# Kernel optimization log

Hardware: AMD Instinct MI355X
Metric: run time of the kernel (lower is better)

Reference implementation:

```python
import jax, jax.numpy as jnp
import numpy as np

N_CLASSES = 18
NMS_PRE = 1000   # test_cfg.nms_pre, per level
K_NMS = 500      # per-class candidates entering greedy NMS
SCORE_THR = 0.01
IOU_THR = 0.5
LEVEL_NS = [600000, 300000, 150000, 75000]


def _decode(points, pred):
    # fcaf3d axis-aligned decode: pred = (dx-, dx+, dy-, dy+, dz-, dz+) >= 0
    cx = points[:, 0] + (pred[:, 1] - pred[:, 0]) / 2
    cy = points[:, 1] + (pred[:, 3] - pred[:, 2]) / 2
    cz = points[:, 2] + (pred[:, 5] - pred[:, 4]) / 2
    w = pred[:, 0] + pred[:, 1]
    l = pred[:, 2] + pred[:, 3]
    h = pred[:, 4] + pred[:, 5]
    return jnp.stack([cx, cy, cz, w, l, h], axis=-1)  # [N, 6]


def _iou3d(b):
    # axis-aligned 3D IoU, b: [K,6] (cx,cy,cz,w,l,h) -> [K,K]
    mn = b[:, :3] - b[:, 3:] / 2
    mx = b[:, :3] + b[:, 3:] / 2
    lt = jnp.maximum(mn[:, None, :], mn[None, :, :])
    rb = jnp.minimum(mx[:, None, :], mx[None, :, :])
    inter = jnp.clip(rb - lt, 0.0).prod(-1)
    vol = jnp.clip(mx - mn, 0.0).prod(-1)
    return inter / (vol[:, None] + vol[None, :] - inter + 1e-6)


def _level(centerness, bbox_pred, cls_score, points):
    # fused score: cls.sigmoid() * centerness.sigmoid()
    scores = jax.nn.sigmoid(cls_score) * jax.nn.sigmoid(centerness)  # [N,C]
    max_scores = scores.max(axis=1)
    _, ids = jax.lax.top_k(max_scores, NMS_PRE)  # per-level prefilter
    bboxes = _decode(points[ids], bbox_pred[ids])  # [NMS_PRE, 6]
    return bboxes, scores[ids]


def _nms_class(boxes, scores):
    # boxes [M,6], scores [M] for one class -> greedy NMS on top K_NMS
    valid = scores > SCORE_THR
    s = jnp.where(valid, scores, -1.0)
    sv, order = jax.lax.top_k(s, K_NMS)  # sorted desc
    b = boxes[order]
    v = sv > SCORE_THR
    iou = _iou3d(b)  # [K,K]
    idx = jnp.arange(K_NMS)

    def body(i, sup):
        alive = jnp.logical_not(sup[i])
        return sup | (alive & (iou[i] > IOU_THR) & (idx > i))

    sup = jax.lax.fori_loop(0, K_NMS, body, jnp.logical_not(v))
    keep = jnp.logical_not(sup) & v
    return b, sv, keep


def _forward(levels):
    mlvl_bboxes, mlvl_scores = [], []
    for (cn, bp, cs, pt) in levels:
        b, s = _level(cn, bp, cs, pt)
        mlvl_bboxes.append(b)
        mlvl_scores.append(s)
    bboxes = jnp.concatenate(mlvl_bboxes)  # [4*NMS_PRE, 6]
    scores = jnp.concatenate(mlvl_scores)  # [4*NMS_PRE, C]
    # per-class NMS (vmap over class dim)
    b, sv, keep = jax.vmap(_nms_class, in_axes=(None, 1))(bboxes, scores)
    labels = jnp.broadcast_to(jnp.arange(N_CLASSES, dtype=jnp.int32)[:, None], sv.shape)
    return (b.reshape(-1, 6), sv.reshape(-1), labels.reshape(-1), keep.reshape(-1))


def setup_inputs() -> dict:
    key = jax.random.key(0)
    out = {}
    for li, n in enumerate(LEVEL_NS):
        k1, k2, k3, k4, key = jax.random.split(key, 5)
        out[f'centerness{li}'] = jax.random.normal(k1, (n, 1), jnp.float32)
        out[f'bbox_pred{li}'] = jax.random.uniform(k2, (n, 6), jnp.float32)  # non-negative distances
        out[f'cls_score{li}'] = jax.random.normal(k3, (n, N_CLASSES), jnp.float32)
        out[f'points{li}'] = jax.random.normal(k4, (n, 3), jnp.float32) * 2.0
    return out


def reference(centerness0, bbox_pred0, cls_score0, points0,
              centerness1, bbox_pred1, cls_score1, points1,
              centerness2, bbox_pred2, cls_score2, points2,
              centerness3, bbox_pred3, cls_score3, points3):
    levels = [
        (centerness0, bbox_pred0, cls_score0, points0),
        (centerness1, bbox_pred1, cls_score1, points1),
        (centerness2, bbox_pred2, cls_score2, points2),
        (centerness3, bbox_pred3, cls_score3, points3),
    ]
    return _forward(levels)
```

## Files before the change

kernel.cpp:

```cpp
#include <hip/hip_runtime.h>
#include <math.h>

#define N_CLASSES 18
#define NMS_PRE   1000
#define K_NMS     500
#define POOL      4000
#define LIST_CAP  2048
#define IOU_THR   0.5f
#define SCORE_THR 0.01f

typedef unsigned long long ull;

struct Ptrs {
  const float* cent[4];
  const float* bbox[4];
  const float* cls[4];
  const float* pts[4];
  int off[4];
  int ntot;
};

__device__ __forceinline__ unsigned int fsort(float f){
  unsigned int b = __float_as_uint(f);
  return (b & 0x80000000u) ? ~b : (b | 0x80000000u);
}
__device__ __forceinline__ float fsort_inv(unsigned int k){
  unsigned int b = (k & 0x80000000u) ? (k & 0x7FFFFFFFu) : ~k;
  return __uint_as_float(b);
}
__device__ __forceinline__ float sigmoidf_(float x){
  return 1.0f / (1.0f + expf(-x));
}
__device__ __forceinline__ int level_of(int f, const Ptrs& P){
  return (f >= P.off[3]) ? 3 : (f >= P.off[2]) ? 2 : (f >= P.off[1]) ? 1 : 0;
}

__device__ __forceinline__ ull cx_keep(ull mine, ull part, bool keep_hi){
  ull mx = mine > part ? mine : part;
  ull mn = mine > part ? part : mine;
  return keep_hi ? mx : mn;
}
__device__ __forceinline__ void cxpair(ull &a, ull &b, bool a_hi){
  ull mx = a > b ? a : b;
  ull mn = a > b ? b : a;
  a = a_hi ? mx : mn;
  b = a_hi ? mn : mx;
}

__global__ void __launch_bounds__(256) init_kernel(unsigned int* hist, unsigned int* state,
                        unsigned int* cnts){
  for (int j = threadIdx.x; j < 4*2048; j += 256) hist[j] = 0u;
  if (threadIdx.x < 4){
    state[2*threadIdx.x]   = 0u;
    state[2*threadIdx.x+1] = NMS_PRE;
    cnts[threadIdx.x]      = 0u;
  }
}

__global__ void __launch_bounds__(256) compute_keys(Ptrs P, unsigned int* keys,
                        unsigned int* hist){
  __shared__ float cls_s[256*19];
  __shared__ unsigned int lh[2048];
  int t = threadIdx.x;
  for (int j = t; j < 2048; j += 256) lh[j] = 0u;
  int f0 = blockIdx.x << 8;
  int f = f0 + t;
  float m = 0.f, cent = 0.f;
  bool valid = f < P.ntot;
  int fl = min(f0 + 255, P.ntot - 1);
  bool uni = (level_of(f0, P) == level_of(fl, P)) && (f0 + 255 < P.ntot);
  int Lb = level_of(f0, P);
  if (uni){
    const float* base = P.cls[Lb] + (size_t)(f0 - P.off[Lb]) * N_CLASSES;
    const float4* base4 = (const float4*)base;
    for (int j = t; j < 256*N_CLASSES/4; j += 256){
      float4 v = base4[j];
      int e = 4*j;
      cls_s[((e  )/18)*19 + ((e  )%18)] = v.x;
      cls_s[((e+1)/18)*19 + ((e+1)%18)] = v.y;
      cls_s[((e+2)/18)*19 + ((e+2)%18)] = v.z;
      cls_s[((e+3)/18)*19 + ((e+3)%18)] = v.w;
    }
    __syncthreads();
    m = cls_s[t*19];
#pragma unroll
    for (int c = 1; c < N_CLASSES; ++c) m = fmaxf(m, cls_s[t*19 + c]);
    cent = P.cent[Lb][f - P.off[Lb]];
  } else {
    __syncthreads();
    if (valid){
      int L = level_of(f, P); int i = f - P.off[L];
      const float* cl = P.cls[L] + (size_t)i * N_CLASSES;
      m = cl[0];
      for (int c = 1; c < N_CLASSES; ++c) m = fmaxf(m, cl[c]);
      cent = P.cent[L][i];
    }
  }
  if (valid){
    float s = sigmoidf_(m) * sigmoidf_(cent);
    unsigned int key = fsort(s);
    keys[f] = key;
    unsigned int bin = key >> 21;
    if (uni) atomicAdd(&lh[bin], 1u);
    else     atomicAdd(&hist[level_of(f, P)*2048 + bin], 1u);
  }
  __syncthreads();
  if (uni){
    for (int j = t; j < 2048; j += 256){
      unsigned int v = lh[j];
      if (v) atomicAdd(&hist[Lb*2048 + j], v);
    }
  }
}

__global__ void __launch_bounds__(256) hist_level(Ptrs P, const unsigned int* keys,
                        const unsigned int* state, unsigned int* hist){
  int f = blockIdx.x * 256 + threadIdx.x;
  if (f < P.ntot){
    int L = level_of(f, P);
    unsigned int key = keys[f];
    unsigned int Pfx = state[2*L];
    if ((key >> 21) == (Pfx >> 21))
      atomicAdd(&hist[L*2048 + ((key >> 10) & 0x7FFu)], 1u);
  }
}

__global__ void __launch_bounds__(256) scan_level(unsigned int* hist, unsigned int* state, int pass){
  __shared__ unsigned int lhist[4*2048];
  int t = threadIdx.x;
  int w = t >> 6, lane = t & 63;
  for (int j = t; j < 4*2048; j += 256) lhist[j] = hist[j];
  __syncthreads();
  {
    unsigned int krem = state[2*w + 1];
    unsigned int Pfx  = state[2*w];
    unsigned int carry = 0;
    for (int ch = 0; ch < 32; ++ch){
      int d = ch*64 + lane;
      unsigned int cnt = lhist[w*2048 + (2047 - d)];
      unsigned int pfx = cnt;
#pragma unroll
      for (int off = 1; off < 64; off <<= 1){
        unsigned int u = __shfl_up(pfx, off);
        if (lane >= off) pfx += u;
      }
      unsigned int C = carry + pfx;
      ull bal = __ballot(C >= krem);
      if (bal){
        int fl2 = __ffsll(bal) - 1;
        unsigned int Cf = __shfl(C, fl2);
        unsigned int cf = __shfl(cnt, fl2);
        if (lane == 0){
          unsigned int b = (unsigned int)(2047 - (ch*64 + fl2));
          state[2*w]     = (pass == 0) ? (b << 21) : (Pfx | (b << 10));
          state[2*w + 1] = krem - (Cf - cf);
        }
        break;
      }
      carry = __shfl(C, 63);
    }
  }
  if (pass == 0){
    __syncthreads();
    for (int j = t; j < 4*2048; j += 256) hist[j] = 0u;
  }
}

__global__ void __launch_bounds__(256) compact_kernel(Ptrs P, const unsigned int* keys,
                        const unsigned int* state, unsigned int* cnts, ull* lists){
  int f = blockIdx.x * 256 + threadIdx.x;
  if (f >= P.ntot) return;
  int L = level_of(f, P);
  unsigned int key = keys[f];
  unsigned int T = state[2*L];
  if (key >= T){
    unsigned int pos = atomicAdd(&cnts[L], 1u);
    if (pos < LIST_CAP){
      unsigned int i = (unsigned int)(f - P.off[L]);
      lists[(size_t)L*LIST_CAP + pos] = ((ull)key << 32) | (ull)(~i);
    }
  }
}

__global__ void __launch_bounds__(1024) sort_idx(const ull* lists,
                        const unsigned int* cnts, unsigned int* sidx){
  __shared__ ull buf[LIST_CAP];
  int L = blockIdx.x;
  int t = threadIdx.x;
  unsigned int cnt = cnts[L]; if (cnt > LIST_CAP) cnt = LIST_CAP;
  const ull* src = lists + (size_t)L*LIST_CAP;
  if (cnt <= 1024u){
    ull v0 = (t < (int)cnt) ? src[t] : 0ull;
    for (int k = 2; k <= 1024; k <<= 1){
      for (int j = k >> 1; j > 0; j >>= 1){
        bool hi0 = (((t & j) == 0) == ((t & k) == 0));
        if (j >= 64){
          __syncthreads();
          buf[t] = v0;
          __syncthreads();
          ull p0 = buf[t ^ j];
          v0 = cx_keep(v0, p0, hi0);
        } else {
          ull p0 = __shfl_xor(v0, j);
          v0 = cx_keep(v0, p0, hi0);
        }
      }
    }
    if (t < NMS_PRE) sidx[L*NMS_PRE + t] = ~((unsigned int)(v0 & 0xFFFFFFFFu));
  } else {
    int e1 = t + 1024;
    ull v0 = (t  < (int)cnt) ? src[t]  : 0ull;
    ull v1 = (e1 < (int)cnt) ? src[e1] : 0ull;
    for (int k = 2; k <= 2048; k <<= 1){
      for (int j = k >> 1; j > 0; j >>= 1){
        bool hi0 = (((t  & j) == 0) == ((t  & k) == 0));
        bool hi1 = (((e1 & j) == 0) == ((e1 & k) == 0));
        if (j >= 1024){
          cxpair(v0, v1, hi0);
        } else if (j >= 64){
          __syncthreads();
          buf[t] = v0; buf[e1] = v1;
          __syncthreads();
          ull p0 = buf[t ^ j];
          ull p1 = buf[e1 ^ j];
          v0 = cx_keep(v0, p0, hi0);
          v1 = cx_keep(v1, p1, hi1);
        } else {
          ull p0 = __shfl_xor(v0, j);
          ull p1 = __shfl_xor(v1, j);
          v0 = cx_keep(v0, p0, hi0);
          v1 = cx_keep(v1, p1, hi1);
        }
      }
    }
    if (t < NMS_PRE) sidx[L*NMS_PRE + t] = ~((unsigned int)(v0 & 0xFFFFFFFFu));
  }
}

__global__ void __launch_bounds__(64) gather_decode(Ptrs P, const unsigned int* sidx,
                        float* boxes_pool, float* scores_pool){
  int r = blockIdx.x*64 + threadIdx.x;
  if (r >= POOL) return;
  int L = r / NMS_PRE;
  unsigned int i = sidx[r];
  const float* bp = P.bbox[L] + (size_t)i * 6;
  const float* pp = P.pts[L]  + (size_t)i * 3;
  float p0 = bp[0], p1 = bp[1], p2 = bp[2], p3 = bp[3], p4 = bp[4], p5 = bp[5];
  float cx = pp[0] + (p1 - p0) * 0.5f;
  float cy = pp[1] + (p3 - p2) * 0.5f;
  float cz = pp[2] + (p5 - p4) * 0.5f;
  float w = p0 + p1, l = p2 + p3, h = p4 + p5;
  float* bo = boxes_pool + (size_t)r * 6;
  bo[0] = cx; bo[1] = cy; bo[2] = cz; bo[3] = w; bo[4] = l; bo[5] = h;
  float cs = sigmoidf_(P.cent[L][i]);
  const float* cl = P.cls[L] + (size_t)i * N_CLASSES;
#pragma unroll
  for (int c = 0; c < N_CLASSES; ++c)
    scores_pool[(size_t)c * POOL + r] = sigmoidf_(cl[c]) * cs;
}

__global__ void __launch_bounds__(1024) class_topk(const float* scores_pool, const float* boxes_pool,
                        float* out, float* aabb){
  __shared__ unsigned int keyS[4096];
  __shared__ ull comp[512];
  __shared__ unsigned int histS[256];
  __shared__ unsigned int wsum[16], wpre[16];
  __shared__ unsigned int sP, sK, sCnt;
  int c = blockIdx.x;
  int t = threadIdx.x;
  int w = t >> 6, lane = t & 63;

  for (int j = t; j < 4096; j += 1024){
    unsigned int k = 0u;
    if (j < POOL){
      float s = scores_pool[(size_t)c*POOL + j];
      float sval = (s > SCORE_THR) ? s : -1.0f;
      k = fsort(sval);
    }
    keyS[j] = k;
  }
  if (t == 0){ sP = 0u; sK = K_NMS; sCnt = 0u; }
  __syncthreads();

  for (int pass = 0; pass < 4; ++pass){
    int shift = 24 - 8*pass;
    if (t < 256) histS[t] = 0u;
    __syncthreads();
    unsigned int Pfx = sP;
    for (int j = t; j < 4096; j += 1024){
      unsigned int k = keyS[j];
      if ((((ull)(k ^ Pfx)) >> (shift + 8)) == 0ull)
        atomicAdd(&histS[(k >> shift) & 0xFFu], 1u);
    }
    __syncthreads();
    if (w == 0){
      unsigned int krem = sK;
      unsigned int carry = 0;
      for (int ch = 0; ch < 4; ++ch){
        unsigned int cnt = histS[255 - (ch*64 + lane)];
        unsigned int pfx = cnt;
#pragma unroll
        for (int off = 1; off < 64; off <<= 1){
          unsigned int u = __shfl_up(pfx, off);
          if (lane >= off) pfx += u;
        }
        unsigned int C = carry + pfx;
        ull bal = __ballot(C >= krem);
        if (bal){
          int fl = __ffsll(bal) - 1;
          unsigned int Cf = __shfl(C, fl);
          unsigned int cf = __shfl(cnt, fl);
          if (lane == 0){
            sP = Pfx | ((unsigned int)(255 - (ch*64 + fl)) << shift);
            sK = krem - (Cf - cf);
          }
          break;
        }
        carry = __shfl(C, 63);
      }
    }
    __syncthreads();
  }
  unsigned int T = sP, need = sK;

  unsigned int loc[4]; unsigned int ct = 0;
#pragma unroll
  for (int q = 0; q < 4; ++q){
    unsigned int k = keyS[4*t + q];
    loc[q] = k;
    ct += (k == T) ? 1u : 0u;
  }
  unsigned int inc = ct;
#pragma unroll
  for (int off = 1; off < 64; off <<= 1){
    unsigned int u = __shfl_up(inc, off);
    if (lane >= off) inc += u;
  }
  if (lane == 63) wsum[w] = inc;
  __syncthreads();
  if (t < 16){
    unsigned int v = wsum[t];
    unsigned int pincl = v;
#pragma unroll
    for (int off = 1; off < 16; off <<= 1){
      unsigned int u = __shfl_up(pincl, off);
      if (t >= off) pincl += u;
    }
    wpre[t] = pincl - v;
  }
  __syncthreads();
  unsigned int excl = wpre[w] + (inc - ct);

#pragma unroll
  for (int q = 0; q < 4; ++q){
    unsigned int k = loc[q];
    bool surv = false;
    if (k > T) surv = true;
    else if (k == T){ surv = (excl < need); excl += 1u; }
    if (surv){
      unsigned int pos = atomicAdd(&sCnt, 1u);
      if (pos < 512)
        comp[pos] = ((ull)k << 32) | (ull)(~(unsigned int)(4*t + q));
    }
  }
  __syncthreads();

  ull v0 = 0ull;
  if (t < 512 && t < (int)sCnt) v0 = comp[t];
  for (int k = 2; k <= 512; k <<= 1){
    for (int j = k >> 1; j > 0; j >>= 1){
      if (j >= 64){
        __syncthreads();
        if (t < 512) comp[t] = v0;
        __syncthreads();
        if (t < 512){
          ull p0 = comp[t ^ j];
          bool hi0 = (((t & j) == 0) == ((t & k) == 0));
          v0 = cx_keep(v0, p0, hi0);
        }
      } else {
        if (t < 512){
          ull p0 = __shfl_xor(v0, j);
          bool hi0 = (((t & j) == 0) == ((t & k) == 0));
          v0 = cx_keep(v0, p0, hi0);
        }
      }
    }
  }

  if (t < K_NMS){
    ull cm = v0;
    unsigned int j = ~((unsigned int)(cm & 0xFFFFFFFFu));
    float sval = fsort_inv((unsigned int)(cm >> 32));
    int o = c*K_NMS + t;
    const float* bp = boxes_pool + (size_t)j * 6;
    float b0 = bp[0], b1 = bp[1], b2 = bp[2], b3 = bp[3], b4 = bp[4], b5 = bp[5];
    float* ob = out + (size_t)o * 6;
    ob[0] = b0; ob[1] = b1; ob[2] = b2; ob[3] = b3; ob[4] = b4; ob[5] = b5;
    out[54000 + o] = sval;
    out[63000 + o] = (float)c;
    float mn0 = b0 - b3*0.5f, mx0 = b0 + b3*0.5f;
    float mn1 = b1 - b4*0.5f, mx1 = b1 + b4*0.5f;
    float mn2 = b2 - b5*0.5f, mx2 = b2 + b5*0.5f;
    float vol = fmaxf(mx0 - mn0, 0.f) * fmaxf(mx1 - mn1, 0.f) * fmaxf(mx2 - mn2, 0.f);
    float* ap = aabb + ((size_t)c*512 + t) * 8;
    ap[0] = mn0; ap[1] = mn1; ap[2] = mn2; ap[3] = mx0; ap[4] = mx1; ap[5] = mx2;
    ap[6] = vol; ap[7] = sval;
  }
}

__global__ void __launch_bounds__(512) nms_mask(const float* aabb, ull* maskG, ull* flagsG){
  __shared__ float smn0[512], smn1[512], smn2[512];
  __shared__ float smx0[512], smx1[512], smx2[512];
  __shared__ float svol[512];
  __shared__ ull rowbuf[64*8];
  int c = blockIdx.y, chunk = blockIdx.x;
  int t = threadIdx.x, w = t >> 6, lane = t & 63;
  float mn0 = 0.f, mn1 = 0.f, mn2 = 0.f, mx0 = 0.f, mx1 = 0.f, mx2 = 0.f, vol = 0.f;
  if (t < K_NMS){
    const float* ap = aabb + ((size_t)c*512 + t) * 8;
    mn0 = ap[0]; mn1 = ap[1]; mn2 = ap[2];
    mx0 = ap[3]; mx1 = ap[4]; mx2 = ap[5]; vol = ap[6];
  }
  smn0[t] = mn0; smn1[t] = mn1; smn2[t] = mn2;
  smx0[t] = mx0; smx1[t] = mx1; smx2[t] = mx2;
  svol[t] = vol;
  __syncthreads();
  int i0 = chunk * 64, i1 = min(i0 + 64, K_NMS);
  for (int i = i0; i < i1; ++i){
    float lt0 = fmaxf(smn0[i], mn0), lt1 = fmaxf(smn1[i], mn1), lt2 = fmaxf(smn2[i], mn2);
    float rb0 = fminf(smx0[i], mx0), rb1 = fminf(smx1[i], mx1), rb2 = fminf(smx2[i], mx2);
    float inter = fmaxf(rb0 - lt0, 0.f) * fmaxf(rb1 - lt1, 0.f) * fmaxf(rb2 - lt2, 0.f);
    float denom = svol[i] + vol - inter + 1e-6f;
    bool s = (t < K_NMS) && (t > i) && (inter / denom > IOU_THR);
    ull m = __ballot(s);
    if (lane == 0){
      maskG[((size_t)c*K_NMS + i)*8 + w] = m;
      rowbuf[(i - i0)*8 + w] = m;
    }
  }
  __syncthreads();
  if (t < 64){
    int r = i0 + t;
    bool nz = false;
    if (r < K_NMS){
      ull o = 0ull;
#pragma unroll
      for (int z = 0; z < 8; ++z) o |= rowbuf[t*8 + z];
      nz = (o != 0ull);
    }
    ull bal = __ballot(nz);
    if (t == 0) flagsG[(size_t)c*8 + chunk] = bal;
  }
}

__global__ void __launch_bounds__(512) nms_greedy(const float* aabb, const ull* maskG,
                        const ull* flagsG, float* keep_out){
  __shared__ ull maskS[K_NMS*8];
  __shared__ ull vbitsS[8], remS[8];
  int c = blockIdx.x, t = threadIdx.x, w = t >> 6, lane = t & 63;
  ull flg[8];
#pragma unroll
  for (int q = 0; q < 8; ++q) flg[q] = flagsG[(size_t)c*8 + q];
  for (int j = t; j < K_NMS*8; j += 512) maskS[j] = maskG[(size_t)c*K_NMS*8 + j];
  float sv = (t < K_NMS) ? aabb[((size_t)c*512 + t)*8 + 7] : -1.0f;
  ull vb = __ballot(sv > SCORE_THR);
  if (lane == 0) vbitsS[w] = vb;
  __syncthreads();
  if (w == 0){
    ull rem[8];
#pragma unroll
    for (int q = 0; q < 8; ++q) rem[q] = ~vbitsS[q];
#pragma unroll
    for (int q = 0; q < 8; ++q){
      ull cand = flg[q] & ~rem[q];
      while (cand){
        int b = __ffsll(cand) - 1;
        int i = q*64 + b;
#pragma unroll
        for (int z = 0; z < 8; ++z) rem[z] |= maskS[i*8 + z];
        ull above = (b < 63) ? (~0ull << (b + 1)) : 0ull;
        cand = flg[q] & ~rem[q] & above;
      }
    }
    if (lane == 0){
#pragma unroll
      for (int q = 0; q < 8; ++q) remS[q] = rem[q];
    }
  }
  __syncthreads();
  if (t < K_NMS)
    keep_out[c*K_NMS + t] = ((remS[t >> 6] >> (t & 63)) & 1ull) ? 0.0f : 1.0f;
}

extern "C" void kernel_launch(void* const* d_in, const int* in_sizes, int n_in,
                              void* d_out, int out_size, void* d_ws, size_t ws_size,
                              hipStream_t stream){
  Ptrs P;
  int off = 0;
  for (int L = 0; L < 4; ++L){
    P.cent[L] = (const float*)d_in[4*L + 0];
    P.bbox[L] = (const float*)d_in[4*L + 1];
    P.cls[L]  = (const float*)d_in[4*L + 2];
    P.pts[L]  = (const float*)d_in[4*L + 3];
    P.off[L]  = off;
    off += in_sizes[4*L + 0];
  }
  P.ntot = off;

  char* w = (char*)d_ws;
  size_t o = 0;
  auto alloc = [&](size_t bytes) -> char* {
    char* p = w + o;
    o = (o + bytes + 255) & ~(size_t)255;
    return p;
  };
  unsigned int* keys        = (unsigned int*)alloc((size_t)P.ntot * 4);
  unsigned int* hist        = (unsigned int*)alloc(4 * 2048 * 4);
  unsigned int* state       = (unsigned int*)alloc(4 * 2 * 4);
  unsigned int* cnts        = (unsigned int*)alloc(4 * 4);
  ull* lists                = (ull*)alloc((size_t)4 * LIST_CAP * 8);
  unsigned int* sidx        = (unsigned int*)alloc((size_t)POOL * 4);
  float* boxes_pool         = (float*)alloc((size_t)POOL * 6 * 4);
  float* scores_pool        = (float*)alloc((size_t)N_CLASSES * POOL * 4);
  float* aabb               = (float*)alloc((size_t)N_CLASSES * 512 * 8 * 4);
  ull* maskG                = (ull*)alloc((size_t)N_CLASSES * K_NMS * 8 * 8);
  ull* flagsG               = (ull*)alloc((size_t)N_CLASSES * 8 * 8);

  float* out = (float*)d_out;
  int grid = (P.ntot + 255) / 256;

  init_kernel<<<1, 256, 0, stream>>>(hist, state, cnts);
  compute_keys<<<grid, 256, 0, stream>>>(P, keys, hist);
  scan_level<<<1, 256, 0, stream>>>(hist, state, 0);
  hist_level<<<grid, 256, 0, stream>>>(P, keys, state, hist);
  scan_level<<<1, 256, 0, stream>>>(hist, state, 1);
  compact_kernel<<<grid, 256, 0, stream>>>(P, keys, state, cnts, lists);
  sort_idx<<<4, 1024, 0, stream>>>(lists, cnts, sidx);
  gather_decode<<<(POOL + 63)/64, 64, 0, stream>>>(P, sidx, boxes_pool, scores_pool);
  class_topk<<<N_CLASSES, 1024, 0, stream>>>(scores_pool, boxes_pool, out, aabb);
  nms_mask<<<dim3(8, N_CLASSES), 512, 0, stream>>>(aabb, maskG, flagsG);
  nms_greedy<<<N_CLASSES, 512, 0, stream>>>(aabb, maskG, flagsG, out + 72000);
}
```

Baseline: 312.7 us.

## Fuse pipeline stages with last-block scans and merge NMS into class top-k kernel

Cuts the launch chain from eleven kernels to five plus a memset. The two radix-scan passes now run inside the histogram kernels, using a last-block-done atomic counter and threadfence. Gather/decode is folded into the per-level sort kernel, and the IoU mask and greedy NMS stages are merged into the per-class top-k kernel using shared memory instead of global mask buffers. compute_keys also moves to 512-thread blocks with a plain float4 copy into unpadded shared memory. The aim is to remove launch gaps and global round-trips, at the cost of serial tail work in the last block and heavier shared-memory use in class_all.

```diff
diff --git a/kernel.cpp b/kernel.cpp
--- a/kernel.cpp
+++ b/kernel.cpp
@@ -47,52 +47,65 @@
   b = a_hi ? mn : mx;
 }
 
-__global__ void __launch_bounds__(256) init_kernel(unsigned int* hist, unsigned int* state,
-                        unsigned int* cnts){
-  for (int j = threadIdx.x; j < 4*2048; j += 256) hist[j] = 0u;
-  if (threadIdx.x < 4){
-    state[2*threadIdx.x]   = 0u;
-    state[2*threadIdx.x+1] = NMS_PRE;
-    cnts[threadIdx.x]      = 0u;
-  }
-}
-
-__global__ void __launch_bounds__(256) compute_keys(Ptrs P, unsigned int* keys,
-                        unsigned int* hist){
-  __shared__ float cls_s[256*19];
-  __shared__ unsigned int lh[2048];
+__device__ __forceinline__ void level_scan(const unsigned int* st, unsigned int* state,
+                                           int pass, int w, int lane){
+  unsigned int krem = (pass == 0) ? (unsigned)NMS_PRE : state[2*w + 1];
+  unsigned int Pfx  = (pass == 0) ? 0u : state[2*w];
+  unsigned int carry = 0;
+  for (int ch = 0; ch < 32; ++ch){
+    unsigned int cnt = st[w*2048 + 2047 - (ch*64 + lane)];
+    unsigned int pfx = cnt;
+#pragma unroll
+    for (int off2 = 1; off2 < 64; off2 <<= 1){
+      unsigned int u = __shfl_up(pfx, off2);
+      if (lane >= off2) pfx += u;
+    }
+    unsigned int C = carry + pfx;
+    ull bal = __ballot(C >= krem);
+    if (bal){
+      int fl2 = __ffsll(bal) - 1;
+      unsigned int Cf = __shfl(C, fl2);
+      unsigned int cf = __shfl(cnt, fl2);
+      if (lane == 0){
+        unsigned int b = (unsigned int)(2047 - (ch*64 + fl2));
+        state[2*w]     = (pass == 0) ? (b << 21) : (Pfx | (b << 10));
+        state[2*w + 1] = krem - (Cf - cf);
+      }
+      return;
+    }
+    carry = __shfl(C, 63);
+  }
+}
+
+__global__ void __launch_bounds__(512) compute_keys(Ptrs P, unsigned int* keys,
+                        unsigned int* hist, unsigned int* state, unsigned int* done){
+  extern __shared__ char smem[];
+  float* cls_s = (float*)smem;
+  unsigned int* lh = (unsigned int*)(smem + 36864);
   int t = threadIdx.x;
-  for (int j = t; j < 2048; j += 256) lh[j] = 0u;
-  int f0 = blockIdx.x << 8;
+  int f0 = blockIdx.x << 9;
   int f = f0 + t;
+  for (int j = t; j < 2048; j += 512) lh[j] = 0u;
+  bool valid = f < P.ntot;
+  int fl = min(f0 + 511, P.ntot - 1);
+  bool uni = (level_of(f0, P) == level_of(fl, P)) && (f0 + 511 < P.ntot);
+  int Lb = level_of(f0, P);
   float m = 0.f, cent = 0.f;
-  bool valid = f < P.ntot;
-  int fl = min(f0 + 255, P.ntot - 1);
-  bool uni = (level_of(f0, P) == level_of(fl, P)) && (f0 + 255 < P.ntot);
-  int Lb = level_of(f0, P);
   if (uni){
-    const float* base = P.cls[Lb] + (size_t)(f0 - P.off[Lb]) * N_CLASSES;
-    const float4* base4 = (const float4*)base;
-    for (int j = t; j < 256*N_CLASSES/4; j += 256){
-      float4 v = base4[j];
-      int e = 4*j;
-      cls_s[((e  )/18)*19 + ((e  )%18)] = v.x;
-      cls_s[((e+1)/18)*19 + ((e+1)%18)] = v.y;
-      cls_s[((e+2)/18)*19 + ((e+2)%18)] = v.z;
-      cls_s[((e+3)/18)*19 + ((e+3)%18)] = v.w;
-    }
+    const float4* base4 = (const float4*)(P.cls[Lb] + (size_t)(f0 - P.off[Lb]) * N_CLASSES);
+    cent = P.cent[Lb][f - P.off[Lb]];
+    for (int j = t; j < 2304; j += 512) ((float4*)cls_s)[j] = base4[j];
     __syncthreads();
-    m = cls_s[t*19];
-#pragma unroll
-    for (int c = 1; c < N_CLASSES; ++c) m = fmaxf(m, cls_s[t*19 + c]);
-    cent = P.cent[Lb][f - P.off[Lb]];
+    m = cls_s[t*18];
+#pragma unroll
+    for (int c2 = 1; c2 < N_CLASSES; ++c2) m = fmaxf(m, cls_s[t*18 + c2]);
   } else {
     __syncthreads();
     if (valid){
       int L = level_of(f, P); int i = f - P.off[L];
       const float* cl = P.cls[L] + (size_t)i * N_CLASSES;
       m = cl[0];
-      for (int c = 1; c < N_CLASSES; ++c) m = fmaxf(m, cl[c]);
+      for (int c2 = 1; c2 < N_CLASSES; ++c2) m = fmaxf(m, cl[c2]);
       cent = P.cent[L][i];
     }
   }
@@ -100,22 +113,33 @@
     float s = sigmoidf_(m) * sigmoidf_(cent);
     unsigned int key = fsort(s);
     keys[f] = key;
-    unsigned int bin = key >> 21;
-    if (uni) atomicAdd(&lh[bin], 1u);
-    else     atomicAdd(&hist[level_of(f, P)*2048 + bin], 1u);
+    if (uni) atomicAdd(&lh[key >> 21], 1u);
+    else     atomicAdd(&hist[level_of(f, P)*2048 + (key >> 21)], 1u);
   }
   __syncthreads();
   if (uni){
-    for (int j = t; j < 2048; j += 256){
+    for (int j = t; j < 2048; j += 512){
       unsigned int v = lh[j];
       if (v) atomicAdd(&hist[Lb*2048 + j], v);
     }
   }
-}
-
-__global__ void __launch_bounds__(256) hist_level(Ptrs P, const unsigned int* keys,
-                        const unsigned int* state, unsigned int* hist){
-  int f = blockIdx.x * 256 + threadIdx.x;
+  __threadfence();
+  __shared__ unsigned int lastS;
+  if (t == 0) lastS = (atomicAdd(done, 1u) == gridDim.x - 1) ? 1u : 0u;
+  __syncthreads();
+  if (!lastS) return;
+  unsigned int* st = (unsigned int*)smem;
+  for (int j = t; j < 8192; j += 512) st[j] = atomicAdd(&hist[j], 0u);
+  __syncthreads();
+  if (t < 256) level_scan(st, state, 0, t >> 6, t & 63);
+  __syncthreads();
+  for (int j = t; j < 8192; j += 512) hist[j] = 0u;
+}
+
+__global__ void __launch_bounds__(256) hist1_scan(Ptrs P, const unsigned int* keys,
+                        unsigned int* state, unsigned int* hist, unsigned int* done2){
+  int t = threadIdx.x;
+  int f = blockIdx.x * 256 + t;
   if (f < P.ntot){
     int L = level_of(f, P);
     unsigned int key = keys[f];
@@ -123,47 +147,15 @@
     if ((key >> 21) == (Pfx >> 21))
       atomicAdd(&hist[L*2048 + ((key >> 10) & 0x7FFu)], 1u);
   }
-}
-
-__global__ void __launch_bounds__(256) scan_level(unsigned int* hist, unsigned int* state, int pass){
-  __shared__ unsigned int lhist[4*2048];
-  int t = threadIdx.x;
-  int w = t >> 6, lane = t & 63;
-  for (int j = t; j < 4*2048; j += 256) lhist[j] = hist[j];
-  __syncthreads();
-  {
-    unsigned int krem = state[2*w + 1];
-    unsigned int Pfx  = state[2*w];
-    unsigned int carry = 0;
-    for (int ch = 0; ch < 32; ++ch){
-      int d = ch*64 + lane;
-      unsigned int cnt = lhist[w*2048 + (2047 - d)];
-      unsigned int pfx = cnt;
-#pragma unroll
-      for (int off = 1; off < 64; off <<= 1){
-        unsigned int u = __shfl_up(pfx, off);
-        if (lane >= off) pfx += u;
-      }
-      unsigned int C = carry + pfx;
-      ull bal = __ballot(C >= krem);
-      if (bal){
-        int fl2 = __ffsll(bal) - 1;
-        unsigned int Cf = __shfl(C, fl2);
-        unsigned int cf = __shfl(cnt, fl2);
-        if (lane == 0){
-          unsigned int b = (unsigned int)(2047 - (ch*64 + fl2));
-          state[2*w]     = (pass == 0) ? (b << 21) : (Pfx | (b << 10));
-          state[2*w + 1] = krem - (Cf - cf);
-        }
-        break;
-      }
-      carry = __shfl(C, 63);
-    }
-  }
-  if (pass == 0){
-    __syncthreads();
-    for (int j = t; j < 4*2048; j += 256) hist[j] = 0u;
-  }
+  __threadfence();
+  __shared__ unsigned int lastS;
+  if (t == 0) lastS = (atomicAdd(done2, 1u) == gridDim.x - 1) ? 1u : 0u;
+  __syncthreads();
+  if (!lastS) return;
+  __shared__ unsigned int st[8192];
+  for (int j = t; j < 8192; j += 256) st[j] = atomicAdd(&hist[j], 0u);
+  __syncthreads();
+  level_scan(st, state, 1, t >> 6, t & 63);
 }
 
 __global__ void __launch_bounds__(256) compact_kernel(Ptrs P, const unsigned int* keys,
@@ -182,15 +174,16 @@
   }
 }
 
-__global__ void __launch_bounds__(1024) sort_idx(const ull* lists,
-                        const unsigned int* cnts, unsigned int* sidx){
+__global__ void __launch_bounds__(1024) sort_gather(Ptrs P, const ull* lists,
+                        const unsigned int* cnts, float* boxes_pool, float* scores_pool){
   __shared__ ull buf[LIST_CAP];
   int L = blockIdx.x;
   int t = threadIdx.x;
   unsigned int cnt = cnts[L]; if (cnt > LIST_CAP) cnt = LIST_CAP;
   const ull* src = lists + (size_t)L*LIST_CAP;
+  ull v0 = 0ull;
   if (cnt <= 1024u){
-    ull v0 = (t < (int)cnt) ? src[t] : 0ull;
+    v0 = (t < (int)cnt) ? src[t] : 0ull;
     for (int k = 2; k <= 1024; k <<= 1){
       for (int j = k >> 1; j > 0; j >>= 1){
         bool hi0 = (((t & j) == 0) == ((t & k) == 0));
@@ -198,19 +191,16 @@
           __syncthreads();
           buf[t] = v0;
           __syncthreads();
-          ull p0 = buf[t ^ j];
-          v0 = cx_keep(v0, p0, hi0);
+          v0 = cx_keep(v0, buf[t ^ j], hi0);
         } else {
-          ull p0 = __shfl_xor(v0, j);
-          v0 = cx_keep(v0, p0, hi0);
-        }
-      }
-    }
-    if (t < NMS_PRE) sidx[L*NMS_PRE + t] = ~((unsigned int)(v0 & 0xFFFFFFFFu));
+          v0 = cx_keep(v0, __shfl_xor(v0, j), hi0);
+        }
+      }
+    }
   } else {
     int e1 = t + 1024;
-    ull v0 = (t  < (int)cnt) ? src[t]  : 0ull;
-    ull v1 = (e1 < (int)cnt) ? src[e1] : 0ull;
+    v0      = (t  < (int)cnt) ? src[t]  : 0ull;
+    ull v1  = (e1 < (int)cnt) ? src[e1] : 0ull;
     for (int k = 2; k <= 2048; k <<= 1){
       for (int j = k >> 1; j > 0; j >>= 1){
         bool hi0 = (((t  & j) == 0) == ((t  & k) == 0));
@@ -226,46 +216,44 @@
           v0 = cx_keep(v0, p0, hi0);
           v1 = cx_keep(v1, p1, hi1);
         } else {
-          ull p0 = __shfl_xor(v0, j);
-          ull p1 = __shfl_xor(v1, j);
-          v0 = cx_keep(v0, p0, hi0);
-          v1 = cx_keep(v1, p1, hi1);
-        }
-      }
-    }
-    if (t < NMS_PRE) sidx[L*NMS_PRE + t] = ~((unsigned int)(v0 & 0xFFFFFFFFu));
-  }
-}
-
-__global__ void __launch_bounds__(64) gather_decode(Ptrs P, const unsigned int* sidx,
-                        float* boxes_pool, float* scores_pool){
-  int r = blockIdx.x*64 + threadIdx.x;
-  if (r >= POOL) return;
-  int L = r / NMS_PRE;
-  unsigned int i = sidx[r];
-  const float* bp = P.bbox[L] + (size_t)i * 6;
-  const float* pp = P.pts[L]  + (size_t)i * 3;
-  float p0 = bp[0], p1 = bp[1], p2 = bp[2], p3 = bp[3], p4 = bp[4], p5 = bp[5];
-  float cx = pp[0] + (p1 - p0) * 0.5f;
-  float cy = pp[1] + (p3 - p2) * 0.5f;
-  float cz = pp[2] + (p5 - p4) * 0.5f;
-  float w = p0 + p1, l = p2 + p3, h = p4 + p5;
-  float* bo = boxes_pool + (size_t)r * 6;
-  bo[0] = cx; bo[1] = cy; bo[2] = cz; bo[3] = w; bo[4] = l; bo[5] = h;
-  float cs = sigmoidf_(P.cent[L][i]);
-  const float* cl = P.cls[L] + (size_t)i * N_CLASSES;
-#pragma unroll
-  for (int c = 0; c < N_CLASSES; ++c)
-    scores_pool[(size_t)c * POOL + r] = sigmoidf_(cl[c]) * cs;
-}
-
-__global__ void __launch_bounds__(1024) class_topk(const float* scores_pool, const float* boxes_pool,
-                        float* out, float* aabb){
+          v0 = cx_keep(v0, __shfl_xor(v0, j), hi0);
+          v1 = cx_keep(v1, __shfl_xor(v1, j), hi1);
+        }
+      }
+    }
+  }
+  if (t < NMS_PRE){
+    unsigned int i = ~((unsigned int)(v0 & 0xFFFFFFFFu));
+    const float* bp = P.bbox[L] + (size_t)i * 6;
+    const float* pp = P.pts[L]  + (size_t)i * 3;
+    float p0 = bp[0], p1 = bp[1], p2 = bp[2], p3 = bp[3], p4 = bp[4], p5 = bp[5];
+    float cx = pp[0] + (p1 - p0) * 0.5f;
+    float cy = pp[1] + (p3 - p2) * 0.5f;
+    float cz = pp[2] + (p5 - p4) * 0.5f;
+    float w = p0 + p1, l = p2 + p3, h = p4 + p5;
+    int r = L * NMS_PRE + t;
+    float* bo = boxes_pool + (size_t)r * 6;
+    bo[0] = cx; bo[1] = cy; bo[2] = cz; bo[3] = w; bo[4] = l; bo[5] = h;
+    float cs = sigmoidf_(P.cent[L][i]);
+    const float* cl = P.cls[L] + (size_t)i * N_CLASSES;
+#pragma unroll
+    for (int c = 0; c < N_CLASSES; ++c)
+      scores_pool[(size_t)c * POOL + r] = sigmoidf_(cl[c]) * cs;
+  }
+}
+
+__global__ void __launch_bounds__(1024) class_all(const float* scores_pool,
+                        const float* boxes_pool, float* out){
   __shared__ unsigned int keyS[4096];
   __shared__ ull comp[512];
   __shared__ unsigned int histS[256];
   __shared__ unsigned int wsum[16], wpre[16];
   __shared__ unsigned int sP, sK, sCnt;
+  __shared__ float smn0[512], smn1[512], smn2[512];
+  __shared__ float smx0[512], smx1[512], smx2[512];
+  __shared__ float svol[512];
+  __shared__ ull maskS[K_NMS*8];
+  __shared__ ull flagRow[8], vbitsS[8], remS[8];
   int c = blockIdx.x;
   int t = threadIdx.x;
   int w = t >> 6, lane = t & 63;
@@ -280,6 +268,7 @@
     keyS[j] = k;
   }
   if (t == 0){ sP = 0u; sK = K_NMS; sCnt = 0u; }
+  if (t < 8) flagRow[t] = 0ull;
   __syncthreads();
 
   for (int pass = 0; pass < 4; ++pass){
@@ -374,24 +363,26 @@
         if (t < 512) comp[t] = v0;
         __syncthreads();
         if (t < 512){
-          ull p0 = comp[t ^ j];
           bool hi0 = (((t & j) == 0) == ((t & k) == 0));
-          v0 = cx_keep(v0, p0, hi0);
+          v0 = cx_keep(v0, comp[t ^ j], hi0);
         }
       } else {
         if (t < 512){
-          ull p0 = __shfl_xor(v0, j);
           bool hi0 = (((t & j) == 0) == ((t & k) == 0));
-          v0 = cx_keep(v0, p0, hi0);
-        }
-      }
-    }
-  }
-
+          v0 = cx_keep(v0, __shfl_xor(v0, j), hi0);
+        }
+      }
+    }
+  }
+
+  float sval = -1.0f;
+  if (t < 512){
+    sval = fsort_inv((unsigned int)(v0 >> 32));
+    smn0[t] = 0.f; smn1[t] = 0.f; smn2[t] = 0.f;
+    smx0[t] = 0.f; smx1[t] = 0.f; smx2[t] = 0.f; svol[t] = 0.f;
+  }
   if (t < K_NMS){
-    ull cm = v0;
-    unsigned int j = ~((unsigned int)(cm & 0xFFFFFFFFu));
-    float sval = fsort_inv((unsigned int)(cm >> 32));
+    unsigned int j = ~((unsigned int)(v0 & 0xFFFFFFFFu));
     int o = c*K_NMS + t;
     const float* bp = boxes_pool + (size_t)j * 6;
     float b0 = bp[0], b1 = bp[1], b2 = bp[2], b3 = bp[3], b4 = bp[4], b5 = bp[5];
@@ -402,85 +393,49 @@
     float mn0 = b0 - b3*0.5f, mx0 = b0 + b3*0.5f;
     float mn1 = b1 - b4*0.5f, mx1 = b1 + b4*0.5f;
     float mn2 = b2 - b5*0.5f, mx2 = b2 + b5*0.5f;
-    float vol = fmaxf(mx0 - mn0, 0.f) * fmaxf(mx1 - mn1, 0.f) * fmaxf(mx2 - mn2, 0.f);
-    float* ap = aabb + ((size_t)c*512 + t) * 8;
-    ap[0] = mn0; ap[1] = mn1; ap[2] = mn2; ap[3] = mx0; ap[4] = mx1; ap[5] = mx2;
-    ap[6] = vol; ap[7] = sval;
-  }
-}
-
-__global__ void __launch_bounds__(512) nms_mask(const float* aabb, ull* maskG, ull* flagsG){
-  __shared__ float smn0[512], smn1[512], smn2[512];
-  __shared__ float smx0[512], smx1[512], smx2[512];
-  __shared__ float svol[512];
-  __shared__ ull rowbuf[64*8];
-  int c = blockIdx.y, chunk = blockIdx.x;
-  int t = threadIdx.x, w = t >> 6, lane = t & 63;
-  float mn0 = 0.f, mn1 = 0.f, mn2 = 0.f, mx0 = 0.f, mx1 = 0.f, mx2 = 0.f, vol = 0.f;
-  if (t < K_NMS){
-    const float* ap = aabb + ((size_t)c*512 + t) * 8;
-    mn0 = ap[0]; mn1 = ap[1]; mn2 = ap[2];
-    mx0 = ap[3]; mx1 = ap[4]; mx2 = ap[5]; vol = ap[6];
-  }
-  smn0[t] = mn0; smn1[t] = mn1; smn2[t] = mn2;
-  smx0[t] = mx0; smx1[t] = mx1; smx2[t] = mx2;
-  svol[t] = vol;
-  __syncthreads();
-  int i0 = chunk * 64, i1 = min(i0 + 64, K_NMS);
-  for (int i = i0; i < i1; ++i){
-    float lt0 = fmaxf(smn0[i], mn0), lt1 = fmaxf(smn1[i], mn1), lt2 = fmaxf(smn2[i], mn2);
-    float rb0 = fminf(smx0[i], mx0), rb1 = fminf(smx1[i], mx1), rb2 = fminf(smx2[i], mx2);
+    smn0[t] = mn0; smn1[t] = mn1; smn2[t] = mn2;
+    smx0[t] = mx0; smx1[t] = mx1; smx2[t] = mx2;
+    svol[t] = fmaxf(mx0 - mn0, 0.f) * fmaxf(mx1 - mn1, 0.f) * fmaxf(mx2 - mn2, 0.f);
+  }
+  ull vb = __ballot(sval > SCORE_THR);
+  if (w < 8 && lane == 0) vbitsS[w] = vb;
+  __syncthreads();
+
+  int tc = t & 511;
+  int gw = w & 7;
+  float cmn0 = smn0[tc], cmn1 = smn1[tc], cmn2 = smn2[tc];
+  float cmx0 = smx0[tc], cmx1 = smx1[tc], cmx2 = smx2[tc];
+  float cvol = svol[tc];
+  for (int it = 0; it < 250; ++it){
+    int i = 2*it + (t >= 512 ? 1 : 0);
+    float lt0 = fmaxf(smn0[i], cmn0), lt1 = fmaxf(smn1[i], cmn1), lt2 = fmaxf(smn2[i], cmn2);
+    float rb0 = fminf(smx0[i], cmx0), rb1 = fminf(smx1[i], cmx1), rb2 = fminf(smx2[i], cmx2);
     float inter = fmaxf(rb0 - lt0, 0.f) * fmaxf(rb1 - lt1, 0.f) * fmaxf(rb2 - lt2, 0.f);
-    float denom = svol[i] + vol - inter + 1e-6f;
-    bool s = (t < K_NMS) && (t > i) && (inter / denom > IOU_THR);
+    float denom = svol[i] + cvol - inter + 1e-6f;
+    bool s = (tc < K_NMS) && (tc > i) && (inter / denom > IOU_THR);
     ull m = __ballot(s);
     if (lane == 0){
-      maskG[((size_t)c*K_NMS + i)*8 + w] = m;
-      rowbuf[(i - i0)*8 + w] = m;
-    }
-  }
-  __syncthreads();
-  if (t < 64){
-    int r = i0 + t;
-    bool nz = false;
-    if (r < K_NMS){
-      ull o = 0ull;
-#pragma unroll
-      for (int z = 0; z < 8; ++z) o |= rowbuf[t*8 + z];
-      nz = (o != 0ull);
-    }
-    ull bal = __ballot(nz);
-    if (t == 0) flagsG[(size_t)c*8 + chunk] = bal;
-  }
-}
-
-__global__ void __launch_bounds__(512) nms_greedy(const float* aabb, const ull* maskG,
-                        const ull* flagsG, float* keep_out){
-  __shared__ ull maskS[K_NMS*8];
-  __shared__ ull vbitsS[8], remS[8];
-  int c = blockIdx.x, t = threadIdx.x, w = t >> 6, lane = t & 63;
-  ull flg[8];
-#pragma unroll
-  for (int q = 0; q < 8; ++q) flg[q] = flagsG[(size_t)c*8 + q];
-  for (int j = t; j < K_NMS*8; j += 512) maskS[j] = maskG[(size_t)c*K_NMS*8 + j];
-  float sv = (t < K_NMS) ? aabb[((size_t)c*512 + t)*8 + 7] : -1.0f;
-  ull vb = __ballot(sv > SCORE_THR);
-  if (lane == 0) vbitsS[w] = vb;
-  __syncthreads();
+      maskS[i*8 + gw] = m;
+      if (m) atomicOr(&flagRow[i >> 6], 1ull << (i & 63));
+    }
+  }
+  __syncthreads();
+
   if (w == 0){
     ull rem[8];
 #pragma unroll
     for (int q = 0; q < 8; ++q) rem[q] = ~vbitsS[q];
 #pragma unroll
     for (int q = 0; q < 8; ++q){
-      ull cand = flg[q] & ~rem[q];
+      ull fq = flagRow[q];
+      ull cand = fq & ~rem[q];
       while (cand){
         int b = __ffsll(cand) - 1;
         int i = q*64 + b;
 #pragma unroll
         for (int z = 0; z < 8; ++z) rem[z] |= maskS[i*8 + z];
         ull above = (b < 63) ? (~0ull << (b + 1)) : 0ull;
-        cand = flg[q] & ~rem[q] & above;
+        cand = fq & ~rem[q] & above;
       }
     }
     if (lane == 0){
@@ -490,7 +445,7 @@
   }
   __syncthreads();
   if (t < K_NMS)
-    keep_out[c*K_NMS + t] = ((remS[t >> 6] >> (t & 63)) & 1ull) ? 0.0f : 1.0f;
+    out[72000 + c*K_NMS + t] = ((remS[t >> 6] >> (t & 63)) & 1ull) ? 0.0f : 1.0f;
 }
 
 extern "C" void kernel_launch(void* const* d_in, const int* in_sizes, int n_in,
@@ -515,30 +470,25 @@
     o = (o + bytes + 255) & ~(size_t)255;
     return p;
   };
-  unsigned int* keys        = (unsigned int*)alloc((size_t)P.ntot * 4);
-  unsigned int* hist        = (unsigned int*)alloc(4 * 2048 * 4);
-  unsigned int* state       = (unsigned int*)alloc(4 * 2 * 4);
-  unsigned int* cnts        = (unsigned int*)alloc(4 * 4);
-  ull* lists                = (ull*)alloc((size_t)4 * LIST_CAP * 8);
-  unsigned int* sidx        = (unsigned int*)alloc((size_t)POOL * 4);
-  float* boxes_pool         = (float*)alloc((size_t)POOL * 6 * 4);
-  float* scores_pool        = (float*)alloc((size_t)N_CLASSES * POOL * 4);
-  float* aabb               = (float*)alloc((size_t)N_CLASSES * 512 * 8 * 4);
-  ull* maskG                = (ull*)alloc((size_t)N_CLASSES * K_NMS * 8 * 8);
-  ull* flagsG               = (ull*)alloc((size_t)N_CLASSES * 8 * 8);
+  unsigned int* keys  = (unsigned int*)alloc((size_t)P.ntot * 4);
+  char* ctrl          = alloc(32768 + 16 + 4 + 4);
+  unsigned int* hist  = (unsigned int*)ctrl;
+  unsigned int* cnts  = (unsigned int*)(ctrl + 32768);
+  unsigned int* done  = (unsigned int*)(ctrl + 32784);
+  unsigned int* done2 = (unsigned int*)(ctrl + 32788);
+  unsigned int* state = (unsigned int*)alloc(4 * 2 * 4);
+  ull* lists          = (ull*)alloc((size_t)4 * LIST_CAP * 8);
+  float* boxes_pool   = (float*)alloc((size_t)POOL * 6 * 4);
+  float* scores_pool  = (float*)alloc((size_t)N_CLASSES * POOL * 4);
 
   float* out = (float*)d_out;
-  int grid = (P.ntot + 255) / 256;
-
-  init_kernel<<<1, 256, 0, stream>>>(hist, state, cnts);
-  compute_keys<<<grid, 256, 0, stream>>>(P, keys, hist);
-  scan_level<<<1, 256, 0, stream>>>(hist, state, 0);
-  hist_level<<<grid, 256, 0, stream>>>(P, keys, state, hist);
-  scan_level<<<1, 256, 0, stream>>>(hist, state, 1);
-  compact_kernel<<<grid, 256, 0, stream>>>(P, keys, state, cnts, lists);
-  sort_idx<<<4, 1024, 0, stream>>>(lists, cnts, sidx);
-  gather_decode<<<(POOL + 63)/64, 64, 0, stream>>>(P, sidx, boxes_pool, scores_pool);
-  class_topk<<<N_CLASSES, 1024, 0, stream>>>(scores_pool, boxes_pool, out, aabb);
-  nms_mask<<<dim3(8, N_CLASSES), 512, 0, stream>>>(aabb, maskG, flagsG);
-  nms_greedy<<<N_CLASSES, 512, 0, stream>>>(aabb, maskG, flagsG, out + 72000);
-}
+  int grid512 = (P.ntot + 511) / 512;
+  int grid256 = (P.ntot + 255) / 256;
+
+  hipMemsetAsync(ctrl, 0, 32768 + 24, stream);
+  compute_keys<<<grid512, 512, 45056, stream>>>(P, keys, hist, state, done);
+  hist1_scan<<<grid256, 256, 0, stream>>>(P, keys, state, hist, done2);
+  compact_kernel<<<grid256, 256, 0, stream>>>(P, keys, state, cnts, lists);
+  sort_gather<<<4, 1024, 0, stream>>>(P, lists, cnts, boxes_pool, scores_pool);
+  class_all<<<N_CLASSES, 1024, 0, stream>>>(scores_pool, boxes_pool, out);
+}
```

Measured after the change: 894.2 us. 186% more time.
